# Kernel optimization log

Hardware: AMD Instinct MI355X
Metric: run time of the kernel (lower is better)

The kernel has to match this reference:

```python
import jax, jax.numpy as jnp
import numpy as np

N_NODES = 100000
N_EDGES = 1600000
IN_F = 256
OUT_F = 64


def setup_inputs() -> dict:
    key = jax.random.key(0)
    k1, k2, k3, k4, k5 = jax.random.split(key, 5)
    features = jax.random.normal(k1, (N_NODES, IN_F), dtype=jnp.float32)
    # xavier_uniform for [in, out] weight
    limit = float(np.sqrt(6.0 / (IN_F + OUT_F)))
    weight = jax.random.uniform(k2, (IN_F, OUT_F), dtype=jnp.float32, minval=-limit, maxval=limit)
    adj_rows = jnp.sort(jax.random.randint(k3, (N_EDGES,), 0, N_NODES, dtype=jnp.int32))
    adj_cols = jax.random.randint(k4, (N_EDGES,), 0, N_NODES, dtype=jnp.int32)
    # positive edge weights (e.g. normalized adjacency values)
    adj_vals = jax.random.uniform(k5, (N_EDGES,), dtype=jnp.float32) * (1.0 / 16.0)
    return {
        "features": features,
        "weight": weight,
        "adj_rows": adj_rows,
        "adj_cols": adj_cols,
        "adj_vals": adj_vals,
        "active": 1,
    }


def _spmm(rows, cols, vals, x, n_nodes):
    # sparse [N,N] @ dense [N,F]: gather neighbor rows, scale, scatter-add
    gathered = vals[:, None] * x[cols]          # [E, F]
    return jax.ops.segment_sum(gathered, rows, num_segments=n_nodes)


def reference(features, weight, adj_rows, adj_cols, adj_vals, active):
    support = features @ weight                 # [N, out]
    if active:
        support = jnp.tanh(support)
    n = features.shape[0]
    output = _spmm(adj_rows, adj_cols, adj_vals, support, n)  # adj @ support
    az = _spmm(adj_rows, adj_cols, adj_vals, output, n)       # adj @ output
    return (output, az)
```

## Files before the change

kernel.cpp:

```cpp
#include <hip/hip_runtime.h>
#include <hip/hip_bf16.h>
#include <math.h>

#define IN_F  256
#define OUT_F 64
#define PD    264

typedef __attribute__((ext_vector_type(8))) short bf16x8;
typedef __attribute__((ext_vector_type(4))) float f32x4;

__device__ inline unsigned short f2b(float x) {
    union { __hip_bfloat16 h; unsigned short u; } cv;
    cv.h = __float2bfloat16(x);
    return cv.u;
}
__device__ inline float b2f_lo(unsigned int u) { return __uint_as_float(u << 16); }
__device__ inline float b2f_hi(unsigned int u) { return __uint_as_float(u & 0xffff0000u); }

__global__ __launch_bounds__(512) void gemm_rowptr_kernel(
    const float* __restrict__ feat,
    const float* __restrict__ w,
    const int*  __restrict__ active,
    const int*  __restrict__ rows,
    unsigned short* __restrict__ sup_bf,
    int* __restrict__ row_ptr,
    int N, int E, int GB)
{
    __shared__ unsigned short wt[OUT_F * PD];

    if ((int)blockIdx.x >= GB) {
        int e = ((int)blockIdx.x - GB) * 512 + (int)threadIdx.x;
        if (e < E) {
            int r  = rows[e];
            int rn = (e + 1 < E) ? rows[e + 1] : N;
            if (e == 0) {
                for (int j = 0; j <= r; ++j) row_ptr[j] = 0;
            }
            for (int j = r + 1; j <= rn; ++j) row_ptr[j] = e + 1;
        }
        return;
    }

    const int t = threadIdx.x;
    #pragma unroll
    for (int r = 0; r < 8; ++r) {
        int f = r * 512 + t;
        float4 v = ((const float4*)w)[f];
        int k = f >> 4;
        int n = (f & 15) << 2;
        wt[(n + 0) * PD + k] = f2b(v.x);
        wt[(n + 1) * PD + k] = f2b(v.y);
        wt[(n + 2) * PD + k] = f2b(v.z);
        wt[(n + 3) * PD + k] = f2b(v.w);
    }
    __syncthreads();

    const int lane = t & 63;
    const int m    = lane & 15;
    const int quad = lane >> 4;
    const int node0 = (int)blockIdx.x * 128 + (t >> 6) * 16;

    int nd = node0 + m;
    if (nd > N - 1) nd = N - 1;
    const float* arow = feat + (size_t)nd * IN_F;

    f32x4 acc[4];
    #pragma unroll
    for (int b = 0; b < 4; ++b) acc[b] = (f32x4)0.0f;

    #pragma unroll
    for (int kt = 0; kt < 8; ++kt) {
        const int ko = kt * 32 + quad * 8;
        f32x4 lo = *(const f32x4*)(arow + ko);
        f32x4 hi = *(const f32x4*)(arow + ko + 4);
        bf16x8 a;
        a[0] = (short)f2b(lo[0]); a[1] = (short)f2b(lo[1]);
        a[2] = (short)f2b(lo[2]); a[3] = (short)f2b(lo[3]);
        a[4] = (short)f2b(hi[0]); a[5] = (short)f2b(hi[1]);
        a[6] = (short)f2b(hi[2]); a[7] = (short)f2b(hi[3]);
        #pragma unroll
        for (int nt = 0; nt < 4; ++nt) {
            bf16x8 b = *(const bf16x8*)(&wt[(nt * 16 + m) * PD + ko]);
            acc[nt] = __builtin_amdgcn_mfma_f32_16x16x32_bf16(a, b, acc[nt], 0, 0, 0);
        }
    }

    int act = __builtin_amdgcn_readfirstlane(active[0]);
    #pragma unroll
    for (int r = 0; r < 4; ++r) {
        int node = node0 + quad * 4 + r;
        if (node >= N) continue;
        #pragma unroll
        for (int nt = 0; nt < 4; ++nt) {
            float v = acc[nt][r];
            if (act) v = tanhf(v);
            sup_bf[(size_t)node * OUT_F + nt * 16 + m] = f2b(v);
        }
    }
}

__device__ inline int lower_bound(const int* __restrict__ a, int n, int key) {
    int lo = 0, hi = n;
    while (lo < hi) {
        int mid = (lo + hi) >> 1;
        if (a[mid] < key) lo = mid + 1; else hi = mid;
    }
    return lo;
}

__device__ __forceinline__ void fma8b(float v, uint4 g, float* acc) {
    acc[0] = fmaf(v, b2f_lo(g.x), acc[0]); acc[1] = fmaf(v, b2f_hi(g.x), acc[1]);
    acc[2] = fmaf(v, b2f_lo(g.y), acc[2]); acc[3] = fmaf(v, b2f_hi(g.y), acc[3]);
    acc[4] = fmaf(v, b2f_lo(g.z), acc[4]); acc[5] = fmaf(v, b2f_hi(g.z), acc[5]);
    acc[6] = fmaf(v, b2f_lo(g.w), acc[6]); acc[7] = fmaf(v, b2f_hi(g.w), acc[7]);
}
__device__ __forceinline__ void fma8f(float v, float4 lo, float4 hi, float* acc) {
    acc[0] = fmaf(v, lo.x, acc[0]); acc[1] = fmaf(v, lo.y, acc[1]);
    acc[2] = fmaf(v, lo.z, acc[2]); acc[3] = fmaf(v, lo.w, acc[3]);
    acc[4] = fmaf(v, hi.x, acc[4]); acc[5] = fmaf(v, hi.y, acc[5]);
    acc[6] = fmaf(v, hi.z, acc[6]); acc[7] = fmaf(v, hi.w, acc[7]);
}

template <bool XBF>
__global__ __launch_bounds__(256) void spmm_kernel(
    const int* __restrict__ row_ptr,
    const int* __restrict__ rows,
    const int* __restrict__ cols,
    const float* __restrict__ vals,
    const void* __restrict__ x,
    float* __restrict__ out,
    unsigned short* __restrict__ out_bf,
    int N, int E)
{
    const int row  = blockIdx.x * 4 + (threadIdx.x >> 6);
    const int lane = threadIdx.x & 63;
    const int part = lane & 7;
    const int esl  = lane >> 3;
    if (row >= N) return;

    int s, e;
    if (row_ptr) { s = row_ptr[row]; e = row_ptr[row + 1]; }
    else         { s = lower_bound(rows, E, row); e = lower_bound(rows, E, row + 1); }

    const unsigned short* xb = (const unsigned short*)x;
    const float*          xf = (const float*)x;

    float acc[8] = {0.f, 0.f, 0.f, 0.f, 0.f, 0.f, 0.f, 0.f};

    int i = s;
    for (; i + 16 <= e; i += 16) {
        int   ea = i + esl,  eb = i + 8 + esl;
        int   ca = cols[ea], cb = cols[eb];
        float va = vals[ea], vb = vals[eb];
        if (XBF) {
            uint4 ga = *(const uint4*)(xb + (size_t)ca * OUT_F + part * 8);
            uint4 gb = *(const uint4*)(xb + (size_t)cb * OUT_F + part * 8);
            fma8b(va, ga, acc);
            fma8b(vb, gb, acc);
        } else {
            const float* pa = xf + (size_t)ca * OUT_F + part * 8;
            const float* pb = xf + (size_t)cb * OUT_F + part * 8;
            float4 la = *(const float4*)pa, ha = *(const float4*)(pa + 4);
            float4 lb = *(const float4*)pb, hb = *(const float4*)(pb + 4);
            fma8f(va, la, ha, acc);
            fma8f(vb, lb, hb, acc);
        }
    }
    if (i < e) {
        int   ea = i + esl, eb = i + 8 + esl;
        float va = 0.f, vb = 0.f;
        if (XBF) {
            uint4 ga = make_uint4(0u, 0u, 0u, 0u);
            uint4 gb = make_uint4(0u, 0u, 0u, 0u);
            if (ea < e) { int c = cols[ea]; va = vals[ea];
                          ga = *(const uint4*)(xb + (size_t)c * OUT_F + part * 8); }
            if (eb < e) { int c = cols[eb]; vb = vals[eb];
                          gb = *(const uint4*)(xb + (size_t)c * OUT_F + part * 8); }
            fma8b(va, ga, acc);
            fma8b(vb, gb, acc);
        } else {
            float4 la = make_float4(0.f,0.f,0.f,0.f), ha = la, lb = la, hb = la;
            if (ea < e) { int c = cols[ea]; va = vals[ea];
                          const float* p = xf + (size_t)c * OUT_F + part * 8;
                          la = *(const float4*)p; ha = *(const float4*)(p + 4); }
            if (eb < e) { int c = cols[eb]; vb = vals[eb];
                          const float* p = xf + (size_t)c * OUT_F + part * 8;
                          lb = *(const float4*)p; hb = *(const float4*)(p + 4); }
            fma8f(va, la, ha, acc);
            fma8f(vb, lb, hb, acc);
        }
    }

    #pragma unroll
    for (int j = 0; j < 8; ++j) {
        acc[j] += __shfl_xor(acc[j], 8, 64);
        acc[j] += __shfl_xor(acc[j], 16, 64);
        acc[j] += __shfl_xor(acc[j], 32, 64);
    }

    if (esl == 0) {
        size_t base = (size_t)row * OUT_F + part * 8;
        f32x4 o0 = {acc[0], acc[1], acc[2], acc[3]};
        f32x4 o1 = {acc[4], acc[5], acc[6], acc[7]};
        __builtin_nontemporal_store(o0, (f32x4*)(out + base));
        __builtin_nontemporal_store(o1, (f32x4*)(out + base + 4));
        if (out_bf) {
            uint4 pk;
            pk.x = (unsigned)f2b(acc[0]) | ((unsigned)f2b(acc[1]) << 16);
            pk.y = (unsigned)f2b(acc[2]) | ((unsigned)f2b(acc[3]) << 16);
            pk.z = (unsigned)f2b(acc[4]) | ((unsigned)f2b(acc[5]) << 16);
            pk.w = (unsigned)f2b(acc[6]) | ((unsigned)f2b(acc[7]) << 16);
            *(uint4*)(out_bf + base) = pk;
        }
    }
}

extern "C" void kernel_launch(void* const* d_in, const int* in_sizes, int n_in,
                              void* d_out, int out_size, void* d_ws, size_t ws_size,
                              hipStream_t stream) {
    const float* feat   = (const float*)d_in[0];
    const float* w      = (const float*)d_in[1];
    const int*   rows   = (const int*)d_in[2];
    const int*   cols   = (const int*)d_in[3];
    const float* vals   = (const float*)d_in[4];
    const int*   active = (const int*)d_in[5];

    const int N = in_sizes[0] / IN_F;
    const int E = in_sizes[2];

    float* out = (float*)d_out;
    float* az  = out + (size_t)N * OUT_F;

    size_t rp_bytes = (((size_t)(N + 1) * sizeof(int)) + 255) & ~(size_t)255;
    size_t bf_bytes = (((size_t)N * OUT_F * sizeof(unsigned short)) + 255) & ~(size_t)255;
    char* ws = (char*)d_ws;

    int* row_ptr = (ws_size >= rp_bytes) ? (int*)ws : nullptr;
    size_t used = row_ptr ? rp_bytes : 0;

    unsigned short* sup_bf;
    unsigned short* mid_bf = nullptr;
    if (ws_size >= used + 2 * bf_bytes) {
        sup_bf = (unsigned short*)(ws + used);
        mid_bf = (unsigned short*)(ws + used + bf_bytes);
    } else if (ws_size >= used + bf_bytes) {
        sup_bf = (unsigned short*)(ws + used);
    } else {
        sup_bf = (unsigned short*)az;
    }

    {
        int GB = (N + 127) / 128;
        int RB = row_ptr ? (E + 511) / 512 : 0;
        gemm_rowptr_kernel<<<GB + RB, 512, 0, stream>>>(
            feat, w, active, rows, sup_bf, row_ptr, N, E, GB);
    }

    int spmm_blocks = (N + 3) / 4;
    spmm_kernel<true><<<spmm_blocks, 256, 0, stream>>>(
        row_ptr, rows, cols, vals, sup_bf, out, mid_bf, N, E);
    if (mid_bf) {
        spmm_kernel<true><<<spmm_blocks, 256, 0, stream>>>(
            row_ptr, rows, cols, vals, mid_bf, az, nullptr, N, E);
    } else {
        spmm_kernel<false><<<spmm_blocks, 256, 0, stream>>>(
            row_ptr, rows, cols, vals, out, az, nullptr, N, E);
    }
}
```

Measured before the change: 270.5 us.

## Remap SpMM to half-wave per row with 16-edge unrolled gathers

The SpMM kernel now gives each row to 32 lanes, each owning two feature columns, instead of 64 lanes splitting edges and columns. Every lane walks all edges of its row, loading the column indices and values for 16 edges at a time with uniform addresses, then issuing 16 independent gathers. This removes the cross-lane shuffle reduction and packs two rows per wave. In exchange each gather is narrower (4 or 8 bytes per lane), and short rows waste unrolled slots. The GEMM feature loads also switch to nontemporal loads.

New measurement: 263.4 us (median of 2 runs). 1.03x faster.

```diff
diff --git a/kernel.cpp b/kernel.cpp
--- a/kernel.cpp
+++ b/kernel.cpp
@@ -8,6 +8,7 @@
 
 typedef __attribute__((ext_vector_type(8))) short bf16x8;
 typedef __attribute__((ext_vector_type(4))) float f32x4;
+typedef __attribute__((ext_vector_type(2))) float f32x2;
 
 __device__ inline unsigned short f2b(float x) {
     union { __hip_bfloat16 h; unsigned short u; } cv;
@@ -71,8 +72,8 @@
     #pragma unroll
     for (int kt = 0; kt < 8; ++kt) {
         const int ko = kt * 32 + quad * 8;
-        f32x4 lo = *(const f32x4*)(arow + ko);
-        f32x4 hi = *(const f32x4*)(arow + ko + 4);
+        f32x4 lo = __builtin_nontemporal_load((const f32x4*)(arow + ko));
+        f32x4 hi = __builtin_nontemporal_load((const f32x4*)(arow + ko + 4));
         bf16x8 a;
         a[0] = (short)f2b(lo[0]); a[1] = (short)f2b(lo[1]);
         a[2] = (short)f2b(lo[2]); a[3] = (short)f2b(lo[3]);
@@ -106,19 +107,6 @@
         if (a[mid] < key) lo = mid + 1; else hi = mid;
     }
     return lo;
-}
-
-__device__ __forceinline__ void fma8b(float v, uint4 g, float* acc) {
-    acc[0] = fmaf(v, b2f_lo(g.x), acc[0]); acc[1] = fmaf(v, b2f_hi(g.x), acc[1]);
-    acc[2] = fmaf(v, b2f_lo(g.y), acc[2]); acc[3] = fmaf(v, b2f_hi(g.y), acc[3]);
-    acc[4] = fmaf(v, b2f_lo(g.z), acc[4]); acc[5] = fmaf(v, b2f_hi(g.z), acc[5]);
-    acc[6] = fmaf(v, b2f_lo(g.w), acc[6]); acc[7] = fmaf(v, b2f_hi(g.w), acc[7]);
-}
-__device__ __forceinline__ void fma8f(float v, float4 lo, float4 hi, float* acc) {
-    acc[0] = fmaf(v, lo.x, acc[0]); acc[1] = fmaf(v, lo.y, acc[1]);
-    acc[2] = fmaf(v, lo.z, acc[2]); acc[3] = fmaf(v, lo.w, acc[3]);
-    acc[4] = fmaf(v, hi.x, acc[4]); acc[5] = fmaf(v, hi.y, acc[5]);
-    acc[6] = fmaf(v, hi.z, acc[6]); acc[7] = fmaf(v, hi.w, acc[7]);
 }
 
 template <bool XBF>
@@ -132,85 +120,58 @@
     unsigned short* __restrict__ out_bf,
     int N, int E)
 {
-    const int row  = blockIdx.x * 4 + (threadIdx.x >> 6);
     const int lane = threadIdx.x & 63;
-    const int part = lane & 7;
-    const int esl  = lane >> 3;
-    if (row >= N) return;
+    const int h    = lane >> 5;
+    const int l    = lane & 31;
+    const int row  = blockIdx.x * 8 + (threadIdx.x >> 6) * 2 + h;
+
+    const bool valid = row < N;
+    const int  rc    = valid ? row : N - 1;
 
     int s, e;
-    if (row_ptr) { s = row_ptr[row]; e = row_ptr[row + 1]; }
-    else         { s = lower_bound(rows, E, row); e = lower_bound(rows, E, row + 1); }
+    if (row_ptr) { s = row_ptr[rc]; e = row_ptr[rc + 1]; }
+    else         { s = lower_bound(rows, E, rc); e = lower_bound(rows, E, rc + 1); }
+    if (!valid) e = s;
 
     const unsigned short* xb = (const unsigned short*)x;
     const float*          xf = (const float*)x;
 
-    float acc[8] = {0.f, 0.f, 0.f, 0.f, 0.f, 0.f, 0.f, 0.f};
-
-    int i = s;
-    for (; i + 16 <= e; i += 16) {
-        int   ea = i + esl,  eb = i + 8 + esl;
-        int   ca = cols[ea], cb = cols[eb];
-        float va = vals[ea], vb = vals[eb];
+    float a0 = 0.0f, a1 = 0.0f;
+
+    for (int base = s; base < e; base += 16) {
+        int   c[16];
+        float v[16];
+        #pragma unroll
+        for (int j = 0; j < 16; ++j) {
+            int idx = base + j;
+            int cl  = idx < e ? idx : e - 1;
+            c[j] = cols[cl];
+            v[j] = (idx < e) ? vals[cl] : 0.0f;
+        }
         if (XBF) {
-            uint4 ga = *(const uint4*)(xb + (size_t)ca * OUT_F + part * 8);
-            uint4 gb = *(const uint4*)(xb + (size_t)cb * OUT_F + part * 8);
-            fma8b(va, ga, acc);
-            fma8b(vb, gb, acc);
+            #pragma unroll
+            for (int j = 0; j < 16; ++j) {
+                unsigned int g = *(const unsigned int*)(xb + (size_t)c[j] * OUT_F + 2 * l);
+                a0 = fmaf(v[j], b2f_lo(g), a0);
+                a1 = fmaf(v[j], b2f_hi(g), a1);
+            }
         } else {
-            const float* pa = xf + (size_t)ca * OUT_F + part * 8;
-            const float* pb = xf + (size_t)cb * OUT_F + part * 8;
-            float4 la = *(const float4*)pa, ha = *(const float4*)(pa + 4);
-            float4 lb = *(const float4*)pb, hb = *(const float4*)(pb + 4);
-            fma8f(va, la, ha, acc);
-            fma8f(vb, lb, hb, acc);
-        }
-    }
-    if (i < e) {
-        int   ea = i + esl, eb = i + 8 + esl;
-        float va = 0.f, vb = 0.f;
-        if (XBF) {
-            uint4 ga = make_uint4(0u, 0u, 0u, 0u);
-            uint4 gb = make_uint4(0u, 0u, 0u, 0u);
-            if (ea < e) { int c = cols[ea]; va = vals[ea];
-                          ga = *(const uint4*)(xb + (size_t)c * OUT_F + part * 8); }
-            if (eb < e) { int c = cols[eb]; vb = vals[eb];
-                          gb = *(const uint4*)(xb + (size_t)c * OUT_F + part * 8); }
-            fma8b(va, ga, acc);
-            fma8b(vb, gb, acc);
-        } else {
-            float4 la = make_float4(0.f,0.f,0.f,0.f), ha = la, lb = la, hb = la;
-            if (ea < e) { int c = cols[ea]; va = vals[ea];
-                          const float* p = xf + (size_t)c * OUT_F + part * 8;
-                          la = *(const float4*)p; ha = *(const float4*)(p + 4); }
-            if (eb < e) { int c = cols[eb]; vb = vals[eb];
-                          const float* p = xf + (size_t)c * OUT_F + part * 8;
-                          lb = *(const float4*)p; hb = *(const float4*)(p + 4); }
-            fma8f(va, la, ha, acc);
-            fma8f(vb, lb, hb, acc);
-        }
-    }
-
-    #pragma unroll
-    for (int j = 0; j < 8; ++j) {
-        acc[j] += __shfl_xor(acc[j], 8, 64);
-        acc[j] += __shfl_xor(acc[j], 16, 64);
-        acc[j] += __shfl_xor(acc[j], 32, 64);
-    }
-
-    if (esl == 0) {
-        size_t base = (size_t)row * OUT_F + part * 8;
-        f32x4 o0 = {acc[0], acc[1], acc[2], acc[3]};
-        f32x4 o1 = {acc[4], acc[5], acc[6], acc[7]};
-        __builtin_nontemporal_store(o0, (f32x4*)(out + base));
-        __builtin_nontemporal_store(o1, (f32x4*)(out + base + 4));
+            #pragma unroll
+            for (int j = 0; j < 16; ++j) {
+                float2 g = *(const float2*)(xf + (size_t)c[j] * OUT_F + 2 * l);
+                a0 = fmaf(v[j], g.x, a0);
+                a1 = fmaf(v[j], g.y, a1);
+            }
+        }
+    }
+
+    if (valid) {
+        size_t bidx = (size_t)row * OUT_F + 2 * l;
+        f32x2 o = {a0, a1};
+        __builtin_nontemporal_store(o, (f32x2*)(out + bidx));
         if (out_bf) {
-            uint4 pk;
-            pk.x = (unsigned)f2b(acc[0]) | ((unsigned)f2b(acc[1]) << 16);
-            pk.y = (unsigned)f2b(acc[2]) | ((unsigned)f2b(acc[3]) << 16);
-            pk.z = (unsigned)f2b(acc[4]) | ((unsigned)f2b(acc[5]) << 16);
-            pk.w = (unsigned)f2b(acc[6]) | ((unsigned)f2b(acc[7]) << 16);
-            *(uint4*)(out_bf + base) = pk;
+            unsigned int pk = (unsigned int)f2b(a0) | ((unsigned int)f2b(a1) << 16);
+            *(unsigned int*)(out_bf + bidx) = pk;
         }
     }
 }
@@ -256,7 +217,7 @@
             feat, w, active, rows, sup_bf, row_ptr, N, E, GB);
     }
 
-    int spmm_blocks = (N + 3) / 4;
+    int spmm_blocks = (N + 7) / 8;
     spmm_kernel<true><<<spmm_blocks, 256, 0, stream>>>(
         row_ptr, rows, cols, vals, sup_bf, out, mid_bf, N, E);
     if (mid_bf) {
```
